# Optimization experiments

Measured on AMD Instinct MI355X. Metric: run time of the kernel, lower is better.

## Reference

```python
import jax, jax.numpy as jnp
import numpy as np

B, T, C, H = 512, 256, 128, 128


def setup_inputs() -> dict:
    key = jax.random.key(0)
    kx, kk, kq, kv = jax.random.split(key, 4)
    x = jax.random.normal(kx, (B, T, C), dtype=jnp.float32)
    # weights stored as [in, out]; Linear(bias=False) is x @ W
    Wk = jax.random.normal(kk, (C, H), dtype=jnp.float32) * 0.02
    Wq = jax.random.normal(kq, (C, H), dtype=jnp.float32) * 0.02
    Wv = jax.random.normal(kv, (C, H), dtype=jnp.float32) * 0.02
    return {"x": x, "Wk": Wk, "Wq": Wq, "Wv": Wv}


def reference(x, Wk, Wq, Wv):
    Bx, Tx, Cx = x.shape
    k = jnp.einsum("btc,ch->bth", x, Wk)
    q = jnp.einsum("btc,ch->bth", x, Wq)
    v = jnp.einsum("btc,ch->bth", x, Wv)
    scale = Cx ** -0.5  # NOTE: original scales by n_embd (C), not head_size
    wei = jnp.einsum("bth,bsh->bts", q, k) * scale  # [B, T, T]
    causal = jnp.tril(jnp.ones((Tx, Tx), dtype=bool))
    wei = jnp.where(causal[None, :, :], wei, -jnp.inf)
    wei = jax.nn.softmax(wei, axis=-1)
    # dropout is identity in eval mode
    out = jnp.einsum("bts,bsh->bth", wei, v)  # [B, T, H]
    return (out, k, v)  # matches (out, present=(k, v))
```

## Files before the change

kernel.cpp:

```cpp
#include <hip/hip_runtime.h>

typedef unsigned short u16;
typedef __attribute__((ext_vector_type(8))) short short8;
typedef __attribute__((ext_vector_type(4))) float float4v;

#define BTH (512*256*128)
#define MASKV (-30000.0f)

__device__ __forceinline__ u16 f2bf(float f){
    union{float f; unsigned i;} v; v.f = f;
    unsigned x = v.i;
    unsigned r = (x + 0x7FFFu + ((x >> 16) & 1u)) >> 16;
    return (u16)r;
}

__global__ void wt_kernel(const float* __restrict__ Wq, const float* __restrict__ Wk,
                          const float* __restrict__ Wv, u16* __restrict__ WT){
    int idx = blockIdx.x * 256 + threadIdx.x;
    int w   = idx >> 14;
    int rem = idx & 16383;
    int n = rem >> 7;
    int k = rem & 127;
    const float* src = (w == 0) ? Wq : (w == 1) ? Wk : Wv;
    float val = src[k * 128 + n];
    if (w == 0) val *= 0.08838834764831845f;
    WT[idx] = f2bf(val);
}

__global__ __launch_bounds__(512, 1) void fused_kernel(const float* __restrict__ x,
                                                       const u16* __restrict__ WT,
                                                       float* __restrict__ dout){
    __shared__ u16 Kbuf [4 * 256 * 32];
    __shared__ u16 VTbuf[8 * 128 * 32];
    __shared__ u16 ps   [8 * 1152];

    int b = blockIdx.x;
    int tid = threadIdx.x;
    int w = tid >> 6, lane = tid & 63, lq = lane & 15, quad = lane >> 4;

    const float* xb   = x    + (size_t)b * 256 * 128;
    float*       oout = dout + (size_t)b * 256 * 128;
    float*       kout = dout + (size_t)BTH     + (size_t)b * 256 * 128;
    float*       vout = dout + (size_t)2 * BTH + (size_t)b * 256 * 128;

    const int rtg[2] = { w, w + 8 };

    short8 ax[2][4];
    #pragma unroll
    for (int rt = 0; rt < 2; rt++){
        #pragma unroll
        for (int ks = 0; ks < 4; ks++){
            const float* px = xb + (size_t)(rtg[rt]*16 + lq)*128 + ks*32 + quad*8;
            float4v lo = *(const float4v*)px;
            float4v hi = *(const float4v*)(px + 4);
            short8 s;
            #pragma unroll
            for (int j = 0; j < 4; j++){
                s[j]     = (short)f2bf(lo[j]);
                s[j + 4] = (short)f2bf(hi[j]);
            }
            ax[rt][ks] = s;
        }
    }

    u16* qs = VTbuf + w * 4096;
    short8 qf[2][4];
    #pragma unroll
    for (int rt = 0; rt < 2; rt++){
        #pragma unroll
        for (int ht = 0; ht < 8; ht++){
            short8 bw[4];
            #pragma unroll
            for (int ks = 0; ks < 4; ks++)
                bw[ks] = *(const short8*)(WT + (size_t)(ht*16 + lq)*128 + ks*32 + quad*8);
            float4v c = {0.f,0.f,0.f,0.f};
            #pragma unroll
            for (int ks = 0; ks < 4; ks++)
                c = __builtin_amdgcn_mfma_f32_16x16x32_bf16(ax[rt][ks], bw[ks], c, 0, 0, 0);
            #pragma unroll
            for (int r = 0; r < 4; r++)
                qs[(quad*4 + r)*136 + ht*16 + lq] = f2bf(c[r]);
        }
        #pragma unroll
        for (int ks = 0; ks < 4; ks++)
            qf[rt][ks] = *(const short8*)(qs + lq*136 + ks*32 + quad*8);
    }
    __syncthreads();

    #pragma unroll
    for (int rt = 0; rt < 2; rt++){
        #pragma unroll
        for (int ht = 0; ht < 8; ht++){
            short8 bw[4];
            #pragma unroll
            for (int ks = 0; ks < 4; ks++)
                bw[ks] = *(const short8*)(WT + (size_t)16384 + (size_t)(ht*16 + lq)*128 + ks*32 + quad*8);
            float4v c = {0.f,0.f,0.f,0.f};
            #pragma unroll
            for (int ks = 0; ks < 4; ks++)
                c = __builtin_amdgcn_mfma_f32_16x16x32_bf16(ax[rt][ks], bw[ks], c, 0, 0, 0);
            #pragma unroll
            for (int r = 0; r < 4; r++){
                int key = rtg[rt]*16 + quad*4 + r;
                kout[(size_t)key*128 + ht*16 + lq] = c[r];
                Kbuf[(ht>>1)*8192 + key*32 + (ht&1)*16 + lq] = f2bf(c[r]);
            }
        }
    }

    #pragma unroll
    for (int ht = 0; ht < 8; ht++){
        short8 bv[4];
        #pragma unroll
        for (int ks = 0; ks < 4; ks++)
            bv[ks] = *(const short8*)(WT + (size_t)2*16384 + (size_t)(ht*16 + lq)*128 + ks*32 + quad*8);
        #pragma unroll
        for (int rt = 0; rt < 2; rt++){
            float4v c = {0.f,0.f,0.f,0.f};
            #pragma unroll
            for (int ks = 0; ks < 4; ks++)
                c = __builtin_amdgcn_mfma_f32_16x16x32_bf16(ax[rt][ks], bv[ks], c, 0, 0, 0);
            #pragma unroll
            for (int r = 0; r < 4; r++)
                vout[(size_t)(rtg[rt]*16 + quad*4 + r)*128 + ht*16 + lq] = c[r];
            float4v ct = {0.f,0.f,0.f,0.f};
            #pragma unroll
            for (int ks = 0; ks < 4; ks++)
                ct = __builtin_amdgcn_mfma_f32_16x16x32_bf16(bv[ks], ax[rt][ks], ct, 0, 0, 0);
            int t = rtg[rt]*16 + lq;
            int e0 = (t>>5)*4096 + (t&31);
            #pragma unroll
            for (int r = 0; r < 4; r++)
                VTbuf[e0 + (ht*16 + quad*4 + r)*32] = f2bf(ct[r]);
        }
    }
    __syncthreads();

    float4v oacc[2][8];
    float mrun[2][4], lrun[2][4];
    #pragma unroll
    for (int rt = 0; rt < 2; rt++){
        #pragma unroll
        for (int o = 0; o < 8; o++) oacc[rt][o] = (float4v){0.f,0.f,0.f,0.f};
        #pragma unroll
        for (int r = 0; r < 4; r++){ mrun[rt][r] = MASKV; lrun[rt][r] = 0.f; }
    }
    u16* psw = ps + w * 1152;

    #pragma unroll
    for (int kb = 0; kb < 4; kb++){
        #pragma unroll
        for (int rt = 0; rt < 2; rt++){
            int rg = rtg[rt];
            if (kb*4 > rg) continue;

            float4v s4[4];
            #pragma unroll
            for (int kt2 = 0; kt2 < 4; kt2++){
                int kt = kb*4 + kt2;
                float4v c = {MASKV, MASKV, MASKV, MASKV};
                if (kt <= rg){
                    c = (float4v){0.f,0.f,0.f,0.f};
                    #pragma unroll
                    for (int ks = 0; ks < 4; ks++){
                        short8 bb = *(const short8*)(Kbuf + ks*8192 + (kt*16 + lq)*32 + quad*8);
                        c = __builtin_amdgcn_mfma_f32_16x16x32_bf16(qf[rt][ks], bb, c, 0, 0, 0);
                    }
                    #pragma unroll
                    for (int r = 0; r < 4; r++)
                        c[r] = fminf(fmaxf(c[r], MASKV), 30000.0f);
                    if (kt == rg){
                        #pragma unroll
                        for (int r = 0; r < 4; r++)
                            if (kt*16 + lq > rg*16 + quad*4 + r) c[r] = MASKV;
                    }
                }
                s4[kt2] = c;
            }
            #pragma unroll
            for (int r = 0; r < 4; r++){
                float mx = fmaxf(fmaxf(s4[0][r], s4[1][r]), fmaxf(s4[2][r], s4[3][r]));
                mx = fmaxf(mx, __shfl_xor(mx, 1));
                mx = fmaxf(mx, __shfl_xor(mx, 2));
                mx = fmaxf(mx, __shfl_xor(mx, 4));
                mx = fmaxf(mx, __shfl_xor(mx, 8));
                float mnew = fmaxf(mrun[rt][r], mx);
                float alpha = __expf(mrun[rt][r] - mnew);
                float rs = 0.f;
                #pragma unroll
                for (int kt2 = 0; kt2 < 4; kt2++){
                    float pv = __expf(s4[kt2][r] - mnew);
                    s4[kt2][r] = pv;
                    rs += pv;
                }
                rs += __shfl_xor(rs, 1);
                rs += __shfl_xor(rs, 2);
                rs += __shfl_xor(rs, 4);
                rs += __shfl_xor(rs, 8);
                lrun[rt][r] = lrun[rt][r] * alpha + rs;
                mrun[rt][r] = mnew;
                #pragma unroll
                for (int o = 0; o < 8; o++) oacc[rt][o][r] *= alpha;
            }
            #pragma unroll
            for (int kt2 = 0; kt2 < 4; kt2++)
                #pragma unroll
                for (int r = 0; r < 4; r++)
                    psw[(quad*4 + r)*72 + kt2*16 + lq] = f2bf(s4[kt2][r]);
            short8 pa0 = *(const short8*)(psw + lq*72 + quad*8);
            short8 pa1 = *(const short8*)(psw + lq*72 + 32 + quad*8);
            #pragma unroll
            for (int k2 = 0; k2 < 2; k2++){
                short8 pa = (k2 == 0) ? pa0 : pa1;
                #pragma unroll
                for (int o = 0; o < 8; o++){
                    short8 vb = *(const short8*)(VTbuf + (kb*2 + k2)*4096 + (o*16 + lq)*32 + quad*8);
                    oacc[rt][o] = __builtin_amdgcn_mfma_f32_16x16x32_bf16(pa, vb, oacc[rt][o], 0, 0, 0);
                }
            }
        }
    }

    #pragma unroll
    for (int rt = 0; rt < 2; rt++){
        #pragma unroll
        for (int r = 0; r < 4; r++){
            float inv = 1.0f / lrun[rt][r];
            int row = rtg[rt]*16 + quad*4 + r;
            #pragma unroll
            for (int o = 0; o < 8; o++)
                oout[(size_t)row*128 + o*16 + lq] = oacc[rt][o][r] * inv;
        }
    }
}

extern "C" void kernel_launch(void* const* d_in, const int* in_sizes, int n_in,
                              void* d_out, int out_size, void* d_ws, size_t ws_size,
                              hipStream_t stream){
    const float* x  = (const float*)d_in[0];
    const float* Wk = (const float*)d_in[1];
    const float* Wq = (const float*)d_in[2];
    const float* Wv = (const float*)d_in[3];
    float* out = (float*)d_out;
    u16* WT = (u16*)d_ws;

    wt_kernel   <<<192, 256, 0, stream>>>(Wq, Wk, Wv, WT);
    fused_kernel<<<512, 512, 0, stream>>>(x, WT, out);
}
```

Before: 324.3 us.

## Use 16 waves per block, one row tile each, with permuted tile assignment

```diff
diff --git a/kernel.cpp b/kernel.cpp
--- a/kernel.cpp
+++ b/kernel.cpp
@@ -27,46 +27,43 @@
     WT[idx] = f2bf(val);
 }
 
-__global__ __launch_bounds__(512, 1) void fused_kernel(const float* __restrict__ x,
-                                                       const u16* __restrict__ WT,
-                                                       float* __restrict__ dout){
+__global__ __launch_bounds__(1024, 4) void fused_kernel(const float* __restrict__ x,
+                                                        const u16* __restrict__ WT,
+                                                        float* __restrict__ dout){
     __shared__ u16 Kbuf [4 * 256 * 32];
     __shared__ u16 VTbuf[8 * 128 * 32];
-    __shared__ u16 ps   [8 * 1152];
+    __shared__ u16 ps   [16 * 1024];
 
     int b = blockIdx.x;
     int tid = threadIdx.x;
     int w = tid >> 6, lane = tid & 63, lq = lane & 15, quad = lane >> 4;
+
+    const int TILE[16] = {0,15,7,8, 14,1,9,6, 2,13,5,10, 12,3,11,4};
+    int rg = TILE[w];
 
     const float* xb   = x    + (size_t)b * 256 * 128;
     float*       oout = dout + (size_t)b * 256 * 128;
     float*       kout = dout + (size_t)BTH     + (size_t)b * 256 * 128;
     float*       vout = dout + (size_t)2 * BTH + (size_t)b * 256 * 128;
 
-    const int rtg[2] = { w, w + 8 };
-
-    short8 ax[2][4];
-    #pragma unroll
-    for (int rt = 0; rt < 2; rt++){
-        #pragma unroll
-        for (int ks = 0; ks < 4; ks++){
-            const float* px = xb + (size_t)(rtg[rt]*16 + lq)*128 + ks*32 + quad*8;
-            float4v lo = *(const float4v*)px;
-            float4v hi = *(const float4v*)(px + 4);
-            short8 s;
-            #pragma unroll
-            for (int j = 0; j < 4; j++){
-                s[j]     = (short)f2bf(lo[j]);
-                s[j + 4] = (short)f2bf(hi[j]);
-            }
-            ax[rt][ks] = s;
-        }
-    }
-
-    u16* qs = VTbuf + w * 4096;
-    short8 qf[2][4];
-    #pragma unroll
-    for (int rt = 0; rt < 2; rt++){
+    short8 ax[4];
+    #pragma unroll
+    for (int ks = 0; ks < 4; ks++){
+        const float* px = xb + (size_t)(rg*16 + lq)*128 + ks*32 + quad*8;
+        float4v lo = *(const float4v*)px;
+        float4v hi = *(const float4v*)(px + 4);
+        short8 s;
+        #pragma unroll
+        for (int j = 0; j < 4; j++){
+            s[j]     = (short)f2bf(lo[j]);
+            s[j + 4] = (short)f2bf(hi[j]);
+        }
+        ax[ks] = s;
+    }
+
+    u16* qs = Kbuf + w * 2048;
+    short8 qf[4];
+    {
         #pragma unroll
         for (int ht = 0; ht < 8; ht++){
             short8 bw[4];
@@ -76,35 +73,32 @@
             float4v c = {0.f,0.f,0.f,0.f};
             #pragma unroll
             for (int ks = 0; ks < 4; ks++)
-                c = __builtin_amdgcn_mfma_f32_16x16x32_bf16(ax[rt][ks], bw[ks], c, 0, 0, 0);
+                c = __builtin_amdgcn_mfma_f32_16x16x32_bf16(ax[ks], bw[ks], c, 0, 0, 0);
             #pragma unroll
             for (int r = 0; r < 4; r++)
-                qs[(quad*4 + r)*136 + ht*16 + lq] = f2bf(c[r]);
-        }
-        #pragma unroll
-        for (int ks = 0; ks < 4; ks++)
-            qf[rt][ks] = *(const short8*)(qs + lq*136 + ks*32 + quad*8);
+                qs[(quad*4 + r)*128 + ht*16 + lq] = f2bf(c[r]);
+        }
+        #pragma unroll
+        for (int ks = 0; ks < 4; ks++)
+            qf[ks] = *(const short8*)(qs + lq*128 + ks*32 + quad*8);
     }
     __syncthreads();
 
     #pragma unroll
-    for (int rt = 0; rt < 2; rt++){
-        #pragma unroll
-        for (int ht = 0; ht < 8; ht++){
-            short8 bw[4];
-            #pragma unroll
-            for (int ks = 0; ks < 4; ks++)
-                bw[ks] = *(const short8*)(WT + (size_t)16384 + (size_t)(ht*16 + lq)*128 + ks*32 + quad*8);
-            float4v c = {0.f,0.f,0.f,0.f};
-            #pragma unroll
-            for (int ks = 0; ks < 4; ks++)
-                c = __builtin_amdgcn_mfma_f32_16x16x32_bf16(ax[rt][ks], bw[ks], c, 0, 0, 0);
-            #pragma unroll
-            for (int r = 0; r < 4; r++){
-                int key = rtg[rt]*16 + quad*4 + r;
-                kout[(size_t)key*128 + ht*16 + lq] = c[r];
-                Kbuf[(ht>>1)*8192 + key*32 + (ht&1)*16 + lq] = f2bf(c[r]);
-            }
+    for (int ht = 0; ht < 8; ht++){
+        short8 bw[4];
+        #pragma unroll
+        for (int ks = 0; ks < 4; ks++)
+            bw[ks] = *(const short8*)(WT + (size_t)16384 + (size_t)(ht*16 + lq)*128 + ks*32 + quad*8);
+        float4v c = {0.f,0.f,0.f,0.f};
+        #pragma unroll
+        for (int ks = 0; ks < 4; ks++)
+            c = __builtin_amdgcn_mfma_f32_16x16x32_bf16(ax[ks], bw[ks], c, 0, 0, 0);
+        #pragma unroll
+        for (int r = 0; r < 4; r++){
+            int key = rg*16 + quad*4 + r;
+            kout[(size_t)key*128 + ht*16 + lq] = c[r];
+            Kbuf[(ht>>1)*8192 + key*32 + (ht&1)*16 + lq] = f2bf(c[r]);
         }
     }
 
@@ -114,123 +108,110 @@
         #pragma unroll
         for (int ks = 0; ks < 4; ks++)
             bv[ks] = *(const short8*)(WT + (size_t)2*16384 + (size_t)(ht*16 + lq)*128 + ks*32 + quad*8);
-        #pragma unroll
-        for (int rt = 0; rt < 2; rt++){
-            float4v c = {0.f,0.f,0.f,0.f};
-            #pragma unroll
-            for (int ks = 0; ks < 4; ks++)
-                c = __builtin_amdgcn_mfma_f32_16x16x32_bf16(ax[rt][ks], bv[ks], c, 0, 0, 0);
-            #pragma unroll
-            for (int r = 0; r < 4; r++)
-                vout[(size_t)(rtg[rt]*16 + quad*4 + r)*128 + ht*16 + lq] = c[r];
-            float4v ct = {0.f,0.f,0.f,0.f};
-            #pragma unroll
-            for (int ks = 0; ks < 4; ks++)
-                ct = __builtin_amdgcn_mfma_f32_16x16x32_bf16(bv[ks], ax[rt][ks], ct, 0, 0, 0);
-            int t = rtg[rt]*16 + lq;
-            int e0 = (t>>5)*4096 + (t&31);
-            #pragma unroll
-            for (int r = 0; r < 4; r++)
-                VTbuf[e0 + (ht*16 + quad*4 + r)*32] = f2bf(ct[r]);
-        }
+        float4v c = {0.f,0.f,0.f,0.f};
+        #pragma unroll
+        for (int ks = 0; ks < 4; ks++)
+            c = __builtin_amdgcn_mfma_f32_16x16x32_bf16(ax[ks], bv[ks], c, 0, 0, 0);
+        #pragma unroll
+        for (int r = 0; r < 4; r++)
+            vout[(size_t)(rg*16 + quad*4 + r)*128 + ht*16 + lq] = c[r];
+        float4v ct = {0.f,0.f,0.f,0.f};
+        #pragma unroll
+        for (int ks = 0; ks < 4; ks++)
+            ct = __builtin_amdgcn_mfma_f32_16x16x32_bf16(bv[ks], ax[ks], ct, 0, 0, 0);
+        int t = rg*16 + lq;
+        int e0 = (t>>5)*4096 + (t&31);
+        #pragma unroll
+        for (int r = 0; r < 4; r++)
+            VTbuf[e0 + (ht*16 + quad*4 + r)*32] = f2bf(ct[r]);
     }
     __syncthreads();
 
-    float4v oacc[2][8];
-    float mrun[2][4], lrun[2][4];
-    #pragma unroll
-    for (int rt = 0; rt < 2; rt++){
-        #pragma unroll
-        for (int o = 0; o < 8; o++) oacc[rt][o] = (float4v){0.f,0.f,0.f,0.f};
-        #pragma unroll
-        for (int r = 0; r < 4; r++){ mrun[rt][r] = MASKV; lrun[rt][r] = 0.f; }
-    }
-    u16* psw = ps + w * 1152;
+    float4v oacc[8];
+    float mrun[4], lrun[4];
+    #pragma unroll
+    for (int o = 0; o < 8; o++) oacc[o] = (float4v){0.f,0.f,0.f,0.f};
+    #pragma unroll
+    for (int r = 0; r < 4; r++){ mrun[r] = MASKV; lrun[r] = 0.f; }
+    u16* psw = ps + w * 1024;
 
     #pragma unroll
     for (int kb = 0; kb < 4; kb++){
-        #pragma unroll
-        for (int rt = 0; rt < 2; rt++){
-            int rg = rtg[rt];
-            if (kb*4 > rg) continue;
-
-            float4v s4[4];
-            #pragma unroll
-            for (int kt2 = 0; kt2 < 4; kt2++){
-                int kt = kb*4 + kt2;
-                float4v c = {MASKV, MASKV, MASKV, MASKV};
-                if (kt <= rg){
-                    c = (float4v){0.f,0.f,0.f,0.f};
-                    #pragma unroll
-                    for (int ks = 0; ks < 4; ks++){
-                        short8 bb = *(const short8*)(Kbuf + ks*8192 + (kt*16 + lq)*32 + quad*8);
-                        c = __builtin_amdgcn_mfma_f32_16x16x32_bf16(qf[rt][ks], bb, c, 0, 0, 0);
-                    }
+        if (kb*4 > rg) continue;
+
+        float4v s4[4];
+        #pragma unroll
+        for (int kt2 = 0; kt2 < 4; kt2++){
+            int kt = kb*4 + kt2;
+            float4v c = {MASKV, MASKV, MASKV, MASKV};
+            if (kt <= rg){
+                c = (float4v){0.f,0.f,0.f,0.f};
+                #pragma unroll
+                for (int ks = 0; ks < 4; ks++){
+                    short8 bb = *(const short8*)(Kbuf + ks*8192 + (kt*16 + lq)*32 + quad*8);
+                    c = __builtin_amdgcn_mfma_f32_16x16x32_bf16(qf[ks], bb, c, 0, 0, 0);
+                }
+                #pragma unroll
+                for (int r = 0; r < 4; r++)
+                    c[r] = fminf(fmaxf(c[r], MASKV), 30000.0f);
+                if (kt == rg){
                     #pragma unroll
                     for (int r = 0; r < 4; r++)
-                        c[r] = fminf(fmaxf(c[r], MASKV), 30000.0f);
-                    if (kt == rg){
-                        #pragma unroll
-                        for (int r = 0; r < 4; r++)
-                            if (kt*16 + lq > rg*16 + quad*4 + r) c[r] = MASKV;
-                    }
-                }
-                s4[kt2] = c;
-            }
-            #pragma unroll
-            for (int r = 0; r < 4; r++){
-                float mx = fmaxf(fmaxf(s4[0][r], s4[1][r]), fmaxf(s4[2][r], s4[3][r]));
-                mx = fmaxf(mx, __shfl_xor(mx, 1));
-                mx = fmaxf(mx, __shfl_xor(mx, 2));
-                mx = fmaxf(mx, __shfl_xor(mx, 4));
-                mx = fmaxf(mx, __shfl_xor(mx, 8));
-                float mnew = fmaxf(mrun[rt][r], mx);
-                float alpha = __expf(mrun[rt][r] - mnew);
-                float rs = 0.f;
-                #pragma unroll
-                for (int kt2 = 0; kt2 < 4; kt2++){
-                    float pv = __expf(s4[kt2][r] - mnew);
-                    s4[kt2][r] = pv;
-                    rs += pv;
-                }
-                rs += __shfl_xor(rs, 1);
-                rs += __shfl_xor(rs, 2);
-                rs += __shfl_xor(rs, 4);
-                rs += __shfl_xor(rs, 8);
-                lrun[rt][r] = lrun[rt][r] * alpha + rs;
-                mrun[rt][r] = mnew;
-                #pragma unroll
-                for (int o = 0; o < 8; o++) oacc[rt][o][r] *= alpha;
-            }
-            #pragma unroll
-            for (int kt2 = 0; kt2 < 4; kt2++)
-                #pragma unroll
-                for (int r = 0; r < 4; r++)
-                    psw[(quad*4 + r)*72 + kt2*16 + lq] = f2bf(s4[kt2][r]);
-            short8 pa0 = *(const short8*)(psw + lq*72 + quad*8);
-            short8 pa1 = *(const short8*)(psw + lq*72 + 32 + quad*8);
-            #pragma unroll
-            for (int k2 = 0; k2 < 2; k2++){
-                short8 pa = (k2 == 0) ? pa0 : pa1;
-                #pragma unroll
-                for (int o = 0; o < 8; o++){
-                    short8 vb = *(const short8*)(VTbuf + (kb*2 + k2)*4096 + (o*16 + lq)*32 + quad*8);
-                    oacc[rt][o] = __builtin_amdgcn_mfma_f32_16x16x32_bf16(pa, vb, oacc[rt][o], 0, 0, 0);
+                        if (kt*16 + lq > rg*16 + quad*4 + r) c[r] = MASKV;
                 }
             }
-        }
-    }
-
-    #pragma unroll
-    for (int rt = 0; rt < 2; rt++){
+            s4[kt2] = c;
+        }
         #pragma unroll
         for (int r = 0; r < 4; r++){
-            float inv = 1.0f / lrun[rt][r];
-            int row = rtg[rt]*16 + quad*4 + r;
-            #pragma unroll
-            for (int o = 0; o < 8; o++)
-                oout[(size_t)row*128 + o*16 + lq] = oacc[rt][o][r] * inv;
-        }
+            float mx = fmaxf(fmaxf(s4[0][r], s4[1][r]), fmaxf(s4[2][r], s4[3][r]));
+            mx = fmaxf(mx, __shfl_xor(mx, 1));
+            mx = fmaxf(mx, __shfl_xor(mx, 2));
+            mx = fmaxf(mx, __shfl_xor(mx, 4));
+            mx = fmaxf(mx, __shfl_xor(mx, 8));
+            float mnew = fmaxf(mrun[r], mx);
+            float alpha = __expf(mrun[r] - mnew);
+            float rs = 0.f;
+            #pragma unroll
+            for (int kt2 = 0; kt2 < 4; kt2++){
+                float pv = __expf(s4[kt2][r] - mnew);
+                s4[kt2][r] = pv;
+                rs += pv;
+            }
+            rs += __shfl_xor(rs, 1);
+            rs += __shfl_xor(rs, 2);
+            rs += __shfl_xor(rs, 4);
+            rs += __shfl_xor(rs, 8);
+            lrun[r] = lrun[r] * alpha + rs;
+            mrun[r] = mnew;
+            #pragma unroll
+            for (int o = 0; o < 8; o++) oacc[o][r] *= alpha;
+        }
+        #pragma unroll
+        for (int kt2 = 0; kt2 < 4; kt2++)
+            #pragma unroll
+            for (int r = 0; r < 4; r++)
+                psw[(quad*4 + r)*64 + kt2*16 + lq] = f2bf(s4[kt2][r]);
+        short8 pa0 = *(const short8*)(psw + lq*64 + quad*8);
+        short8 pa1 = *(const short8*)(psw + lq*64 + 32 + quad*8);
+        #pragma unroll
+        for (int k2 = 0; k2 < 2; k2++){
+            short8 pa = (k2 == 0) ? pa0 : pa1;
+            #pragma unroll
+            for (int o = 0; o < 8; o++){
+                short8 vb = *(const short8*)(VTbuf + (kb*2 + k2)*4096 + (o*16 + lq)*32 + quad*8);
+                oacc[o] = __builtin_amdgcn_mfma_f32_16x16x32_bf16(pa, vb, oacc[o], 0, 0, 0);
+            }
+        }
+    }
+
+    #pragma unroll
+    for (int r = 0; r < 4; r++){
+        float inv = 1.0f / lrun[r];
+        int row = rg*16 + quad*4 + r;
+        #pragma unroll
+        for (int o = 0; o < 8; o++)
+            oout[(size_t)row*128 + o*16 + lq] = oacc[o][r] * inv;
     }
 }
 
@@ -244,6 +225,6 @@
     float* out = (float*)d_out;
     u16* WT = (u16*)d_ws;
 
-    wt_kernel   <<<192, 256, 0, stream>>>(Wq, Wk, Wv, WT);
-    fused_kernel<<<512, 512, 0, stream>>>(x, WT, out);
-}
+    wt_kernel   <<<192,  256, 0, stream>>>(Wq, Wk, Wv, WT);
+    fused_kernel<<<512, 1024, 0, stream>>>(x, WT, out);
+}
```

After: 323.0 us. About the same (-0.4%).

## Balance causal work across waves and use single-pass full-row softmax

Applied to the files above, without the earlier changes.

```diff
diff --git a/kernel.cpp b/kernel.cpp
--- a/kernel.cpp
+++ b/kernel.cpp
@@ -12,6 +12,12 @@
     unsigned x = v.i;
     unsigned r = (x + 0x7FFFu + ((x >> 16) & 1u)) >> 16;
     return (u16)r;
+}
+
+__device__ __forceinline__ void bar_lds(){
+    asm volatile("s_waitcnt lgkmcnt(0)" ::: "memory");
+    __builtin_amdgcn_sched_barrier(0);
+    __builtin_amdgcn_s_barrier();
 }
 
 __global__ void wt_kernel(const float* __restrict__ Wq, const float* __restrict__ Wk,
@@ -38,30 +44,26 @@
     int tid = threadIdx.x;
     int w = tid >> 6, lane = tid & 63, lq = lane & 15, quad = lane >> 4;
 
+    const int rtg[2] = { w, 15 - w };
+
     const float* xb   = x    + (size_t)b * 256 * 128;
     float*       oout = dout + (size_t)b * 256 * 128;
     float*       kout = dout + (size_t)BTH     + (size_t)b * 256 * 128;
     float*       vout = dout + (size_t)2 * BTH + (size_t)b * 256 * 128;
 
-    const int rtg[2] = { w, w + 8 };
-
     short8 ax[2][4];
     #pragma unroll
-    for (int rt = 0; rt < 2; rt++){
+    for (int rt = 0; rt < 2; rt++)
         #pragma unroll
         for (int ks = 0; ks < 4; ks++){
             const float* px = xb + (size_t)(rtg[rt]*16 + lq)*128 + ks*32 + quad*8;
             float4v lo = *(const float4v*)px;
-            float4v hi = *(const float4v*)(px + 4);
+            float4v hv = *(const float4v*)(px + 4);
             short8 s;
             #pragma unroll
-            for (int j = 0; j < 4; j++){
-                s[j]     = (short)f2bf(lo[j]);
-                s[j + 4] = (short)f2bf(hi[j]);
-            }
+            for (int j = 0; j < 4; j++){ s[j] = (short)f2bf(lo[j]); s[j+4] = (short)f2bf(hv[j]); }
             ax[rt][ks] = s;
         }
-    }
 
     u16* qs = VTbuf + w * 4096;
     short8 qf[2][4];
@@ -85,16 +87,16 @@
         for (int ks = 0; ks < 4; ks++)
             qf[rt][ks] = *(const short8*)(qs + lq*136 + ks*32 + quad*8);
     }
-    __syncthreads();
-
-    #pragma unroll
-    for (int rt = 0; rt < 2; rt++){
-        #pragma unroll
-        for (int ht = 0; ht < 8; ht++){
-            short8 bw[4];
-            #pragma unroll
-            for (int ks = 0; ks < 4; ks++)
-                bw[ks] = *(const short8*)(WT + (size_t)16384 + (size_t)(ht*16 + lq)*128 + ks*32 + quad*8);
+    bar_lds();
+
+    #pragma unroll
+    for (int ht = 0; ht < 8; ht++){
+        short8 bw[4];
+        #pragma unroll
+        for (int ks = 0; ks < 4; ks++)
+            bw[ks] = *(const short8*)(WT + (size_t)16384 + (size_t)(ht*16 + lq)*128 + ks*32 + quad*8);
+        #pragma unroll
+        for (int rt = 0; rt < 2; rt++){
             float4v c = {0.f,0.f,0.f,0.f};
             #pragma unroll
             for (int ks = 0; ks < 4; ks++)
@@ -128,33 +130,23 @@
             for (int ks = 0; ks < 4; ks++)
                 ct = __builtin_amdgcn_mfma_f32_16x16x32_bf16(bv[ks], ax[rt][ks], ct, 0, 0, 0);
             int t = rtg[rt]*16 + lq;
-            int e0 = (t>>5)*4096 + (t&31);
             #pragma unroll
             for (int r = 0; r < 4; r++)
-                VTbuf[e0 + (ht*16 + quad*4 + r)*32] = f2bf(ct[r]);
-        }
-    }
-    __syncthreads();
-
-    float4v oacc[2][8];
-    float mrun[2][4], lrun[2][4];
+                VTbuf[(t>>5)*4096 + (ht*16 + quad*4 + r)*32 + (t&31)] = f2bf(ct[r]);
+        }
+    }
+    bar_lds();
+
+    u16* psw = ps + w * 1152;
     #pragma unroll
     for (int rt = 0; rt < 2; rt++){
-        #pragma unroll
-        for (int o = 0; o < 8; o++) oacc[rt][o] = (float4v){0.f,0.f,0.f,0.f};
-        #pragma unroll
-        for (int r = 0; r < 4; r++){ mrun[rt][r] = MASKV; lrun[rt][r] = 0.f; }
-    }
-    u16* psw = ps + w * 1152;
-
-    #pragma unroll
-    for (int kb = 0; kb < 4; kb++){
-        #pragma unroll
-        for (int rt = 0; rt < 2; rt++){
-            int rg = rtg[rt];
-            if (kb*4 > rg) continue;
-
-            float4v s4[4];
+        int rg = rtg[rt];
+        int nch = (rg >> 2) + 1;
+
+        float4v s[4][4];
+        #pragma unroll
+        for (int kb = 0; kb < 4; kb++){
+            if (kb >= nch) continue;
             #pragma unroll
             for (int kt2 = 0; kt2 < 4; kt2++){
                 int kt = kb*4 + kt2;
@@ -172,41 +164,55 @@
                     if (kt == rg){
                         #pragma unroll
                         for (int r = 0; r < 4; r++)
-                            if (kt*16 + lq > rg*16 + quad*4 + r) c[r] = MASKV;
+                            if (lq > quad*4 + r) c[r] = MASKV;
                     }
                 }
-                s4[kt2] = c;
-            }
-            #pragma unroll
-            for (int r = 0; r < 4; r++){
-                float mx = fmaxf(fmaxf(s4[0][r], s4[1][r]), fmaxf(s4[2][r], s4[3][r]));
-                mx = fmaxf(mx, __shfl_xor(mx, 1));
-                mx = fmaxf(mx, __shfl_xor(mx, 2));
-                mx = fmaxf(mx, __shfl_xor(mx, 4));
-                mx = fmaxf(mx, __shfl_xor(mx, 8));
-                float mnew = fmaxf(mrun[rt][r], mx);
-                float alpha = __expf(mrun[rt][r] - mnew);
-                float rs = 0.f;
+                s[kb][kt2] = c;
+            }
+        }
+        float lsum[4];
+        #pragma unroll
+        for (int r = 0; r < 4; r++){
+            float mx = MASKV;
+            #pragma unroll
+            for (int kb = 0; kb < 4; kb++){
+                if (kb >= nch) continue;
+                #pragma unroll
+                for (int kt2 = 0; kt2 < 4; kt2++)
+                    mx = fmaxf(mx, s[kb][kt2][r]);
+            }
+            mx = fmaxf(mx, __shfl_xor(mx, 1));
+            mx = fmaxf(mx, __shfl_xor(mx, 2));
+            mx = fmaxf(mx, __shfl_xor(mx, 4));
+            mx = fmaxf(mx, __shfl_xor(mx, 8));
+            float rs = 0.f;
+            #pragma unroll
+            for (int kb = 0; kb < 4; kb++){
+                if (kb >= nch) continue;
                 #pragma unroll
                 for (int kt2 = 0; kt2 < 4; kt2++){
-                    float pv = __expf(s4[kt2][r] - mnew);
-                    s4[kt2][r] = pv;
+                    float pv = __expf(s[kb][kt2][r] - mx);
+                    s[kb][kt2][r] = pv;
                     rs += pv;
                 }
-                rs += __shfl_xor(rs, 1);
-                rs += __shfl_xor(rs, 2);
-                rs += __shfl_xor(rs, 4);
-                rs += __shfl_xor(rs, 8);
-                lrun[rt][r] = lrun[rt][r] * alpha + rs;
-                mrun[rt][r] = mnew;
-                #pragma unroll
-                for (int o = 0; o < 8; o++) oacc[rt][o][r] *= alpha;
-            }
+            }
+            rs += __shfl_xor(rs, 1);
+            rs += __shfl_xor(rs, 2);
+            rs += __shfl_xor(rs, 4);
+            rs += __shfl_xor(rs, 8);
+            lsum[r] = rs;
+        }
+        float4v oacc[8];
+        #pragma unroll
+        for (int o = 0; o < 8; o++) oacc[o] = (float4v){0.f,0.f,0.f,0.f};
+        #pragma unroll
+        for (int kb = 0; kb < 4; kb++){
+            if (kb >= nch) continue;
             #pragma unroll
             for (int kt2 = 0; kt2 < 4; kt2++)
                 #pragma unroll
                 for (int r = 0; r < 4; r++)
-                    psw[(quad*4 + r)*72 + kt2*16 + lq] = f2bf(s4[kt2][r]);
+                    psw[(quad*4 + r)*72 + kt2*16 + lq] = f2bf(s[kb][kt2][r]);
             short8 pa0 = *(const short8*)(psw + lq*72 + quad*8);
             short8 pa1 = *(const short8*)(psw + lq*72 + 32 + quad*8);
             #pragma unroll
@@ -215,21 +221,17 @@
                 #pragma unroll
                 for (int o = 0; o < 8; o++){
                     short8 vb = *(const short8*)(VTbuf + (kb*2 + k2)*4096 + (o*16 + lq)*32 + quad*8);
-                    oacc[rt][o] = __builtin_amdgcn_mfma_f32_16x16x32_bf16(pa, vb, oacc[rt][o], 0, 0, 0);
+                    oacc[o] = __builtin_amdgcn_mfma_f32_16x16x32_bf16(pa, vb, oacc[o], 0, 0, 0);
                 }
             }
         }
-    }
-
-    #pragma unroll
-    for (int rt = 0; rt < 2; rt++){
         #pragma unroll
         for (int r = 0; r < 4; r++){
-            float inv = 1.0f / lrun[rt][r];
-            int row = rtg[rt]*16 + quad*4 + r;
+            float inv = 1.0f / lsum[r];
+            int row = rg*16 + quad*4 + r;
             #pragma unroll
             for (int o = 0; o < 8; o++)
-                oout[(size_t)row*128 + o*16 + lq] = oacc[rt][o][r] * inv;
+                oout[(size_t)row*128 + o*16 + lq] = oacc[o][r] * inv;
         }
     }
 }
```

After: 314.9 us. -2.9%, faster.
